# Kernel optimization log

Measured on AMD Instinct MI355X. Metric: run time of the kernel, lower is better.

The kernel has to match this reference:

```python
import jax, jax.numpy as jnp
import numpy as np

N_NODES = 100000
N_EDGES = 3200000
F_IN = 512
HIDDEN = 16
N_LABELS = 64


def _degree_norms(edge_src, edge_dst, n):
    # DGL GraphConv norm='both': src side uses out-degree, dst side uses in-degree,
    # both clamped to min 1, raised to -1/2.
    ones = jnp.ones(edge_src.shape[0], dtype=jnp.float32)
    deg_out = jax.ops.segment_sum(ones, edge_src, num_segments=n)
    deg_in = jax.ops.segment_sum(ones, edge_dst, num_segments=n)
    norm_src = jax.lax.rsqrt(jnp.maximum(deg_out, 1.0))
    norm_dst = jax.lax.rsqrt(jnp.maximum(deg_in, 1.0))
    return norm_src, norm_dst


def setup_inputs() -> dict:
    key = jax.random.key(0)
    k_x, k_s, k_d, k_w1, k_b1, k_w2, k_b2 = jax.random.split(key, 7)
    features = jax.random.normal(k_x, (N_NODES, F_IN), dtype=jnp.float32)
    edge_src = jax.random.randint(k_s, (N_EDGES,), 0, N_NODES, dtype=jnp.int64)
    edge_dst = jax.random.randint(k_d, (N_EDGES,), 0, N_NODES, dtype=jnp.int64)
    # GraphConv params (glorot-ish scale)
    W1 = jax.random.normal(k_w1, (F_IN, HIDDEN), dtype=jnp.float32) * (1.0 / np.sqrt(F_IN))
    b1 = jnp.zeros((HIDDEN,), dtype=jnp.float32)
    W2 = jax.random.normal(k_w2, (HIDDEN, N_LABELS), dtype=jnp.float32) * (1.0 / np.sqrt(HIDDEN))
    b2 = jnp.zeros((N_LABELS,), dtype=jnp.float32)
    return {"features": features, "W1": W1, "b1": b1, "W2": W2, "b2": b2,
            "edge_src": edge_src, "edge_dst": edge_dst}


def reference(features, W1, b1, W2, b2, edge_src, edge_dst):
    n = features.shape[0]
    norm_src, norm_dst = _degree_norms(edge_src, edge_dst, n)

    # Layer 1: in_feats (512) > out_feats (16) -> DGL projects first, then aggregates.
    h = features * norm_src[:, None]          # [N, 512]
    h = h @ W1                                 # [N, 16]
    h = jax.ops.segment_sum(h[edge_src], edge_dst, num_segments=n)  # SpMM gather+scatter
    h = h * norm_dst[:, None] + b1
    h = jax.nn.relu(h)  # GraphConv activation; outer F.relu is idempotent

    # Layer 2: in_feats (16) <= out_feats (64) -> DGL aggregates first, then projects.
    h2 = h * norm_src[:, None]                 # [N, 16]
    h2 = jax.ops.segment_sum(h2[edge_src], edge_dst, num_segments=n)
    h2 = h2 * norm_dst[:, None]
    out = h2 @ W2 + b2                          # [N, 64]
    return out
```

## Files before the change

### kernel.cpp

```cpp
#include <hip/hip_runtime.h>

#define N_NODES 100000
#define N_EDGES 3200000
#define F_IN 512
#define HIDDEN 16
#define N_LABELS 64

#define BW 128
#define NBUCK ((N_NODES + BW - 1) / BW)
#define NCB 256
#define SCAN_N (NBUCK * NCB)
#define SCAN_BLKS ((SCAN_N + 1023) / 1024)
#define CAP 10240

__global__ __launch_bounds__(256) void count_kernel(
        const int* __restrict__ es, const int* __restrict__ ed,
        int* __restrict__ Msrc, int* __restrict__ Mdst) {
    __shared__ int h1[NBUCK], h2[NBUCK];
    const int tid = threadIdx.x, g = blockIdx.x;
    for (int i = tid; i < NBUCK; i += 256) { h1[i] = 0; h2[i] = 0; }
    __syncthreads();
    for (int i = g * 256 + tid; i < N_EDGES; i += NCB * 256) {
        atomicAdd(&h1[es[i] >> 7], 1);
        atomicAdd(&h2[ed[i] >> 7], 1);
    }
    __syncthreads();
    for (int i = tid; i < NBUCK; i += 256) {
        Msrc[i * NCB + g] = h1[i];
        Mdst[i * NCB + g] = h2[i];
    }
}

__global__ __launch_bounds__(256) void scanA_kernel(int* __restrict__ a, int* __restrict__ bsum) {
    __shared__ int s[256];
    const int tid = threadIdx.x;
    const int base = blockIdx.x * 1024 + tid * 4;
    int4 v = make_int4(0, 0, 0, 0);
    if (base + 3 < SCAN_N) v = *(const int4*)(a + base);
    else {
        if (base + 0 < SCAN_N) v.x = a[base + 0];
        if (base + 1 < SCAN_N) v.y = a[base + 1];
        if (base + 2 < SCAN_N) v.z = a[base + 2];
        if (base + 3 < SCAN_N) v.w = a[base + 3];
    }
    const int lsum = v.x + v.y + v.z + v.w;
    s[tid] = lsum;
    __syncthreads();
    for (int off = 1; off < 256; off <<= 1) {
        int t = (tid >= off) ? s[tid - off] : 0;
        __syncthreads();
        s[tid] += t;
        __syncthreads();
    }
    int e0 = s[tid] - lsum;
    int e1 = e0 + v.x, e2 = e1 + v.y, e3 = e2 + v.z;
    if (base + 3 < SCAN_N) *(int4*)(a + base) = make_int4(e0, e1, e2, e3);
    else {
        if (base + 0 < SCAN_N) a[base + 0] = e0;
        if (base + 1 < SCAN_N) a[base + 1] = e1;
        if (base + 2 < SCAN_N) a[base + 2] = e2;
        if (base + 3 < SCAN_N) a[base + 3] = e3;
    }
    if (tid == 255) bsum[blockIdx.x] = s[255];
}

__global__ void scanB_kernel(int* __restrict__ bsum) {
    __shared__ int s[256];
    const int tid = threadIdx.x;
    int v = (tid < SCAN_BLKS) ? bsum[tid] : 0;
    s[tid] = v;
    __syncthreads();
    for (int off = 1; off < 256; off <<= 1) {
        int t = (tid >= off) ? s[tid - off] : 0;
        __syncthreads();
        s[tid] += t;
        __syncthreads();
    }
    if (tid < SCAN_BLKS) bsum[tid] = s[tid] - v;
}

__global__ __launch_bounds__(256) void scanC_kernel(int* __restrict__ a, const int* __restrict__ bsum) {
    const int base = blockIdx.x * 1024 + threadIdx.x * 4;
    const int b = bsum[blockIdx.x];
    if (base + 3 < SCAN_N) {
        int4 v = *(int4*)(a + base);
        v.x += b; v.y += b; v.z += b; v.w += b;
        *(int4*)(a + base) = v;
    } else {
        for (int j = 0; j < 4; ++j) if (base + j < SCAN_N) a[base + j] += b;
    }
}

__global__ __launch_bounds__(256) void scatter_kernel(
        const int* __restrict__ es, const int* __restrict__ ed,
        const int* __restrict__ Ssrc, const int* __restrict__ Sdst,
        unsigned* __restrict__ pairs, unsigned char* __restrict__ srcb) {
    __shared__ int c1[NBUCK], c2[NBUCK];
    const int tid = threadIdx.x, g = blockIdx.x;
    for (int i = tid; i < NBUCK; i += 256) {
        c1[i] = Ssrc[i * NCB + g];
        c2[i] = Sdst[i * NCB + g];
    }
    __syncthreads();
    for (int i = g * 256 + tid; i < N_EDGES; i += NCB * 256) {
        int s = es[i], d = ed[i];
        int p2 = atomicAdd(&c2[d >> 7], 1);
        pairs[p2] = ((unsigned)(d & 127) << 17) | (unsigned)s;
        int p1 = atomicAdd(&c1[s >> 7], 1);
        srcb[p1] = (unsigned char)(s & 127);
    }
}

__global__ __launch_bounds__(256) void csr_kernel(
        const int* __restrict__ Sdst, unsigned* __restrict__ pairs,
        int* __restrict__ row_ptr, float* __restrict__ norm_dst) {
    __shared__ unsigned buf[CAP];
    __shared__ int hist[BW], scn[BW], cur[BW];
    const int b = blockIdx.x, tid = threadIdx.x;
    const int base  = Sdst[b * NCB];
    const int nextb = (b == NBUCK - 1) ? N_EDGES : Sdst[(b + 1) * NCB];
    const int nb = nextb - base;
    const bool fits = (nb <= CAP);
    if (tid < BW) hist[tid] = 0;
    __syncthreads();
    for (int i = tid; i < nb; i += 256) {
        unsigned pk = pairs[base + i];
        if (fits) buf[i] = pk;
        atomicAdd(&hist[pk >> 17], 1);
    }
    __syncthreads();
    if (tid < BW) scn[tid] = hist[tid];
    __syncthreads();
    for (int off = 1; off < BW; off <<= 1) {
        int t = 0;
        if (tid < BW && tid >= off) t = scn[tid - off];
        __syncthreads();
        if (tid < BW) scn[tid] += t;
        __syncthreads();
    }
    if (tid < BW) {
        int e = scn[tid] - hist[tid];
        cur[tid] = e;
        int node = b * BW + tid;
        if (node <= N_NODES) row_ptr[node] = base + e;
        if (node < N_NODES) norm_dst[node] = rsqrtf(fmaxf((float)hist[tid], 1.0f));
    }
    __syncthreads();
    if (fits) {
        for (int i = tid; i < nb; i += 256) {
            unsigned pk = buf[i];
            int pos = atomicAdd(&cur[pk >> 17], 1);
            pairs[base + pos] = pk & 0x1FFFFu;
        }
    } else {
        for (int i = tid; i < nb; i += 256)
            pairs[base + i] &= 0x1FFFFu;
    }
}

__global__ __launch_bounds__(256) void srcdeg_kernel(
        const int* __restrict__ Ssrc, const unsigned char* __restrict__ srcb,
        float* __restrict__ norm_src) {
    __shared__ int hist[BW];
    const int b = blockIdx.x, tid = threadIdx.x;
    const int base  = Ssrc[b * NCB];
    const int nextb = (b == NBUCK - 1) ? N_EDGES : Ssrc[(b + 1) * NCB];
    const int nb = nextb - base;
    if (tid < BW) hist[tid] = 0;
    __syncthreads();
    for (int i = tid; i < nb; i += 256)
        atomicAdd(&hist[srcb[base + i]], 1);
    __syncthreads();
    if (tid < BW) {
        int node = b * BW + tid;
        if (node < N_NODES) norm_src[node] = rsqrtf(fmaxf((float)hist[tid], 1.0f));
    }
}

#define P1_ROWS 256
#define P1_CH 32
#define KSPLIT 2
#define KH (F_IN / KSPLIT)
#define P1_CHUNKS (KH / P1_CH)
#define P1_BLKS ((N_NODES + P1_ROWS - 1) / P1_ROWS)

#define GLD16(gp, lp) __builtin_amdgcn_global_load_lds( \
    (const __attribute__((address_space(1))) unsigned int*)(gp), \
    (__attribute__((address_space(3))) unsigned int*)(lp), 16, 0, 0)

__global__ __launch_bounds__(256, 2) void proj1_kernel(
        const float* __restrict__ X, const float* __restrict__ W1,
        float* __restrict__ P0, float* __restrict__ P1) {
    __shared__ float xs[2][P1_ROWS * P1_CH];
    __shared__ float w1c[KH * HIDDEN];

    const int tid = threadIdx.x;
    const int node0 = blockIdx.x * P1_ROWS;
    const int z = blockIdx.y;

    const int srow0 = tid >> 3;
    const int scg   = tid & 7;
    const int wbase = tid & 192;

    for (int i = tid; i < KH * HIDDEN / 4; i += 256)
        ((float4*)w1c)[i] = ((const float4*)(W1 + (size_t)z * KH * HIDDEN))[i];

    {
        const float* Xc = X + (size_t)z * KH;
#pragma unroll
        for (int it = 0; it < 8; ++it) {
            int row = srow0 + it * 32;
            int grow = node0 + row;
            if (grow > N_NODES - 1) grow = N_NODES - 1;
            int cg = scg ^ ((row >> 2) & 7);
            const float* gp = Xc + (size_t)grow * F_IN + cg * 4;
            float* lp = &xs[0][(size_t)(it * 256 + wbase) * 4];
            GLD16(gp, lp);
        }
    }
    __syncthreads();

    const int rg = tid >> 2;
    const int kq = (tid & 3) * 4;

    float acc[4][4];
#pragma unroll
    for (int a = 0; a < 4; ++a)
#pragma unroll
        for (int b = 0; b < 4; ++b) acc[a][b] = 0.f;

    for (int cc = 0; cc < P1_CHUNKS; ++cc) {
        const int cur = cc & 1;

        if (cc + 1 < P1_CHUNKS) {
            const float* Xc = X + (size_t)z * KH + (size_t)(cc + 1) * P1_CH;
#pragma unroll
            for (int it = 0; it < 8; ++it) {
                int row = srow0 + it * 32;
                int grow = node0 + row;
                if (grow > N_NODES - 1) grow = N_NODES - 1;
                int cg = scg ^ ((row >> 2) & 7);
                const float* gp = Xc + (size_t)grow * F_IN + cg * 4;
                float* lp = &xs[cur ^ 1][(size_t)(it * 256 + wbase) * 4];
                GLD16(gp, lp);
            }
        }

        const float* xb = &xs[cur][0];
#pragma unroll
        for (int kk4 = 0; kk4 < 8; ++kk4) {
            float4 w0 = *((const float4*)&w1c[(cc * P1_CH + kk4 * 4 + 0) * HIDDEN + kq]);
            float4 w1 = *((const float4*)&w1c[(cc * P1_CH + kk4 * 4 + 1) * HIDDEN + kq]);
            float4 w2 = *((const float4*)&w1c[(cc * P1_CH + kk4 * 4 + 2) * HIDDEN + kq]);
            float4 w3 = *((const float4*)&w1c[(cc * P1_CH + kk4 * 4 + 3) * HIDDEN + kq]);
#pragma unroll
            for (int a = 0; a < 4; ++a) {
                int row = rg * 4 + a;
                int sw  = (row >> 2) & 7;
                float4 xv = *((const float4*)&xb[row * P1_CH + ((kk4 ^ sw) * 4)]);
                acc[a][0] += xv.x * w0.x; acc[a][1] += xv.x * w0.y;
                acc[a][2] += xv.x * w0.z; acc[a][3] += xv.x * w0.w;
                acc[a][0] += xv.y * w1.x; acc[a][1] += xv.y * w1.y;
                acc[a][2] += xv.y * w1.z; acc[a][3] += xv.y * w1.w;
                acc[a][0] += xv.z * w2.x; acc[a][1] += xv.z * w2.y;
                acc[a][2] += xv.z * w2.z; acc[a][3] += xv.z * w2.w;
                acc[a][0] += xv.w * w3.x; acc[a][1] += xv.w * w3.y;
                acc[a][2] += xv.w * w3.z; acc[a][3] += xv.w * w3.w;
            }
        }

        __syncthreads();
    }

    float* Pz = z ? P1 : P0;
#pragma unroll
    for (int a = 0; a < 4; ++a) {
        int gn = node0 + rg * 4 + a;
        if (gn < N_NODES)
            *((float4*)(Pz + (size_t)gn * HIDDEN + kq)) =
                make_float4(acc[a][0], acc[a][1], acc[a][2], acc[a][3]);
    }
}

__global__ void reduce1_kernel(const float* __restrict__ P0, const float* __restrict__ P1,
                               const float* __restrict__ norm_src, float* __restrict__ H1) {
    int gid = blockIdx.x * blockDim.x + threadIdx.x;
    if (gid < N_NODES * 4) {
        float4 a = ((const float4*)P0)[gid];
        float4 b = ((const float4*)P1)[gid];
        float ns = norm_src[gid >> 2];
        ((float4*)H1)[gid] = make_float4((a.x + b.x) * ns, (a.y + b.y) * ns,
                                         (a.z + b.z) * ns, (a.w + b.w) * ns);
    }
}

__global__ __launch_bounds__(256) void spmm1_kernel(
        const int* __restrict__ rp, const int* __restrict__ col,
        const float* __restrict__ H1, const float* __restrict__ norm_dst,
        const float* __restrict__ norm_src, const float* __restrict__ b1,
        float* __restrict__ H1b) {
    int tid = threadIdx.x;
    int node = blockIdx.x * 16 + (tid >> 4);
    int k = tid & 15;
    if (node >= N_NODES) return;
    int beg = rp[node], end = rp[node + 1];
    float acc = 0.f;
    int j = beg;
    for (; j + 3 < end; j += 4) {
        int s0 = col[j], s1 = col[j + 1], s2 = col[j + 2], s3 = col[j + 3];
        float v0 = H1[(size_t)s0 * HIDDEN + k];
        float v1 = H1[(size_t)s1 * HIDDEN + k];
        float v2 = H1[(size_t)s2 * HIDDEN + k];
        float v3 = H1[(size_t)s3 * HIDDEN + k];
        acc += v0 + v1 + v2 + v3;
    }
    for (; j < end; ++j) acc += H1[(size_t)col[j] * HIDDEN + k];
    float v = fmaxf(acc * norm_dst[node] + b1[k], 0.f) * norm_src[node];
    H1b[(size_t)node * HIDDEN + k] = v;
}

__global__ __launch_bounds__(256) void spmm2_final_kernel(
        const int* __restrict__ rp, const int* __restrict__ col,
        const float* __restrict__ H1b, const float* __restrict__ norm_dst,
        const float* __restrict__ W2, const float* __restrict__ b2,
        float* __restrict__ out) {
    __shared__ float w2s[HIDDEN * N_LABELS];
    int tid = threadIdx.x;
    ((float4*)w2s)[tid] = ((const float4*)W2)[tid];
    __syncthreads();

    int node = blockIdx.x * 16 + (tid >> 4);
    int k = tid & 15;
    if (node >= N_NODES) return;
    int beg = rp[node], end = rp[node + 1];
    float acc = 0.f;
    int j = beg;
    for (; j + 3 < end; j += 4) {
        int s0 = col[j], s1 = col[j + 1], s2 = col[j + 2], s3 = col[j + 3];
        float v0 = H1b[(size_t)s0 * HIDDEN + k];
        float v1 = H1b[(size_t)s1 * HIDDEN + k];
        float v2 = H1b[(size_t)s2 * HIDDEN + k];
        float v3 = H1b[(size_t)s3 * HIDDEN + k];
        acc += v0 + v1 + v2 + v3;
    }
    for (; j < end; ++j) acc += H1b[(size_t)col[j] * HIDDEN + k];
    acc *= norm_dst[node];

    float4 o = ((const float4*)b2)[k];
#pragma unroll
    for (int jj = 0; jj < HIDDEN; ++jj) {
        float hj = __shfl(acc, jj, 16);
        float4 w = *((const float4*)&w2s[jj * N_LABELS + 4 * k]);
        o.x += hj * w.x; o.y += hj * w.y; o.z += hj * w.z; o.w += hj * w.w;
    }
    ((float4*)out)[(size_t)node * 16 + k] = o;
}

extern "C" void kernel_launch(void* const* d_in, const int* in_sizes, int n_in,
                              void* d_out, int out_size, void* d_ws, size_t ws_size,
                              hipStream_t stream) {
    const float* X  = (const float*)d_in[0];
    const float* W1 = (const float*)d_in[1];
    const float* b1 = (const float*)d_in[2];
    const float* W2 = (const float*)d_in[3];
    const float* b2 = (const float*)d_in[4];
    const int* es   = (const int*)d_in[5];
    const int* ed   = (const int*)d_in[6];
    float* out = (float*)d_out;

    char* ws = (char*)d_ws;
    float* norm_src = (float*)ws;  ws += (size_t)N_NODES * 4;
    float* norm_dst = (float*)ws;  ws += (size_t)N_NODES * 4;
    int*   row_ptr  = (int*)ws;    ws += 400016;
    char*  R1 = ws;                ws += (size_t)N_NODES * HIDDEN * 4;
    char*  R2 = ws;                ws += (size_t)N_NODES * HIDDEN * 4;
    char*  R3 = ws;

    unsigned char* srcb = (unsigned char*)R1;
    float* P0  = (float*)R1;
    float* H1  = (float*)R1;
    int*   Sdst = (int*)R2;
    int*   Ssrc = (int*)(R2 + 800768);
    int*   bs1  = (int*)(R2 + 1601536);
    int*   bs2  = (int*)(R2 + 1602560);
    float* P1   = (float*)R2;
    float* H1b  = (float*)R2;
    unsigned* pairs = (unsigned*)R3;
    int*   col  = (int*)R3;

    count_kernel<<<NCB, 256, 0, stream>>>(es, ed, Ssrc, Sdst);
    scanA_kernel<<<SCAN_BLKS, 256, 0, stream>>>(Sdst, bs1);
    scanA_kernel<<<SCAN_BLKS, 256, 0, stream>>>(Ssrc, bs2);
    scanB_kernel<<<1, 256, 0, stream>>>(bs1);
    scanB_kernel<<<1, 256, 0, stream>>>(bs2);
    scanC_kernel<<<SCAN_BLKS, 256, 0, stream>>>(Sdst, bs1);
    scanC_kernel<<<SCAN_BLKS, 256, 0, stream>>>(Ssrc, bs2);
    scatter_kernel<<<NCB, 256, 0, stream>>>(es, ed, Ssrc, Sdst, pairs, srcb);
    csr_kernel<<<NBUCK, 256, 0, stream>>>(Sdst, pairs, row_ptr, norm_dst);
    srcdeg_kernel<<<NBUCK, 256, 0, stream>>>(Ssrc, srcb, norm_src);
    proj1_kernel<<<dim3(P1_BLKS, KSPLIT), 256, 0, stream>>>(X, W1, P0, P1);
    reduce1_kernel<<<(N_NODES * 4 + 255) / 256, 256, 0, stream>>>(P0, P1, norm_src, H1);
    spmm1_kernel<<<(N_NODES + 15) / 16, 256, 0, stream>>>(row_ptr, col, H1, norm_dst, norm_src, b1, H1b);
    spmm2_final_kernel<<<(N_NODES + 15) / 16, 256, 0, stream>>>(row_ptr, col, H1b, norm_dst, W2, b2, out);
}
```

Baseline: 598.8 us.

## Merge scan launches, widen histogram blocks, retile projection to 128 rows x 64 cols

Pairs of scan kernels for the src and dst histograms are merged into single launches using a second grid dimension, cutting launch count. Count and scatter kernels move to 512 threads per block. The first-layer projection is retiled to 128 rows per block with 64-column chunks, two rows per thread and a new swizzle, doubling the grid and skipping the final barrier. Fewer rows per thread lowers register pressure but halves weight reuse per thread, and the scatter ordering within each bucket changes.

```diff
diff --git a/kernel.cpp b/kernel.cpp
--- a/kernel.cpp
+++ b/kernel.cpp
@@ -13,25 +13,29 @@
 #define SCAN_BLKS ((SCAN_N + 1023) / 1024)
 #define CAP 10240
 
-__global__ __launch_bounds__(256) void count_kernel(
+__global__ __launch_bounds__(512) void count_kernel(
         const int* __restrict__ es, const int* __restrict__ ed,
         int* __restrict__ Msrc, int* __restrict__ Mdst) {
     __shared__ int h1[NBUCK], h2[NBUCK];
     const int tid = threadIdx.x, g = blockIdx.x;
-    for (int i = tid; i < NBUCK; i += 256) { h1[i] = 0; h2[i] = 0; }
-    __syncthreads();
-    for (int i = g * 256 + tid; i < N_EDGES; i += NCB * 256) {
+    for (int i = tid; i < NBUCK; i += 512) { h1[i] = 0; h2[i] = 0; }
+    __syncthreads();
+    for (int i = g * 512 + tid; i < N_EDGES; i += NCB * 512) {
         atomicAdd(&h1[es[i] >> 7], 1);
         atomicAdd(&h2[ed[i] >> 7], 1);
     }
     __syncthreads();
-    for (int i = tid; i < NBUCK; i += 256) {
+    for (int i = tid; i < NBUCK; i += 512) {
         Msrc[i * NCB + g] = h1[i];
         Mdst[i * NCB + g] = h2[i];
     }
 }
 
-__global__ __launch_bounds__(256) void scanA_kernel(int* __restrict__ a, int* __restrict__ bsum) {
+__global__ __launch_bounds__(256) void scanA_kernel(
+        int* __restrict__ a0, int* __restrict__ a1,
+        int* __restrict__ b0, int* __restrict__ b1) {
+    int* a    = blockIdx.y ? a1 : a0;
+    int* bsum = blockIdx.y ? b1 : b0;
     __shared__ int s[256];
     const int tid = threadIdx.x;
     const int base = blockIdx.x * 1024 + tid * 4;
@@ -64,7 +68,8 @@
     if (tid == 255) bsum[blockIdx.x] = s[255];
 }
 
-__global__ void scanB_kernel(int* __restrict__ bsum) {
+__global__ void scanB_kernel(int* __restrict__ b0, int* __restrict__ b1) {
+    int* bsum = blockIdx.y ? b1 : b0;
     __shared__ int s[256];
     const int tid = threadIdx.x;
     int v = (tid < SCAN_BLKS) ? bsum[tid] : 0;
@@ -79,7 +84,11 @@
     if (tid < SCAN_BLKS) bsum[tid] = s[tid] - v;
 }
 
-__global__ __launch_bounds__(256) void scanC_kernel(int* __restrict__ a, const int* __restrict__ bsum) {
+__global__ __launch_bounds__(256) void scanC_kernel(
+        int* __restrict__ a0, int* __restrict__ a1,
+        const int* __restrict__ b0, const int* __restrict__ b1) {
+    int* a = blockIdx.y ? a1 : a0;
+    const int* bsum = blockIdx.y ? b1 : b0;
     const int base = blockIdx.x * 1024 + threadIdx.x * 4;
     const int b = bsum[blockIdx.x];
     if (base + 3 < SCAN_N) {
@@ -91,18 +100,18 @@
     }
 }
 
-__global__ __launch_bounds__(256) void scatter_kernel(
+__global__ __launch_bounds__(512) void scatter_kernel(
         const int* __restrict__ es, const int* __restrict__ ed,
         const int* __restrict__ Ssrc, const int* __restrict__ Sdst,
         unsigned* __restrict__ pairs, unsigned char* __restrict__ srcb) {
     __shared__ int c1[NBUCK], c2[NBUCK];
     const int tid = threadIdx.x, g = blockIdx.x;
-    for (int i = tid; i < NBUCK; i += 256) {
+    for (int i = tid; i < NBUCK; i += 512) {
         c1[i] = Ssrc[i * NCB + g];
         c2[i] = Sdst[i * NCB + g];
     }
     __syncthreads();
-    for (int i = g * 256 + tid; i < N_EDGES; i += NCB * 256) {
+    for (int i = g * 512 + tid; i < N_EDGES; i += NCB * 512) {
         int s = es[i], d = ed[i];
         int p2 = atomicAdd(&c2[d >> 7], 1);
         pairs[p2] = ((unsigned)(d & 127) << 17) | (unsigned)s;
@@ -177,8 +186,8 @@
     }
 }
 
-#define P1_ROWS 256
-#define P1_CH 32
+#define P1_ROWS 128
+#define P1_CH 64
 #define KSPLIT 2
 #define KH (F_IN / KSPLIT)
 #define P1_CHUNKS (KH / P1_CH)
@@ -187,6 +196,22 @@
 #define GLD16(gp, lp) __builtin_amdgcn_global_load_lds( \
     (const __attribute__((address_space(1))) unsigned int*)(gp), \
     (__attribute__((address_space(3))) unsigned int*)(lp), 16, 0, 0)
+
+__device__ __forceinline__ void p1_stage(const float* __restrict__ Xz,
+                                         int node0, int cc, float* lbuf,
+                                         int tid) {
+    const int wbase = tid & 192;
+#pragma unroll
+    for (int it = 0; it < 8; ++it) {
+        int row = it * 16 + (tid >> 4);
+        int grow = node0 + row;
+        if (grow > N_NODES - 1) grow = N_NODES - 1;
+        int cg = (tid & 15) ^ ((row >> 1) & 7);
+        const float* gp = Xz + (size_t)grow * F_IN + cc * P1_CH + cg * 4;
+        float* lp = lbuf + (size_t)(it * 256 + wbase) * 4;
+        GLD16(gp, lp);
+    }
+}
 
 __global__ __launch_bounds__(256, 2) void proj1_kernel(
         const float* __restrict__ X, const float* __restrict__ W1,
@@ -197,67 +222,40 @@
     const int tid = threadIdx.x;
     const int node0 = blockIdx.x * P1_ROWS;
     const int z = blockIdx.y;
-
-    const int srow0 = tid >> 3;
-    const int scg   = tid & 7;
-    const int wbase = tid & 192;
+    const float* Xz = X + (size_t)z * KH;
 
     for (int i = tid; i < KH * HIDDEN / 4; i += 256)
         ((float4*)w1c)[i] = ((const float4*)(W1 + (size_t)z * KH * HIDDEN))[i];
 
-    {
-        const float* Xc = X + (size_t)z * KH;
-#pragma unroll
-        for (int it = 0; it < 8; ++it) {
-            int row = srow0 + it * 32;
-            int grow = node0 + row;
-            if (grow > N_NODES - 1) grow = N_NODES - 1;
-            int cg = scg ^ ((row >> 2) & 7);
-            const float* gp = Xc + (size_t)grow * F_IN + cg * 4;
-            float* lp = &xs[0][(size_t)(it * 256 + wbase) * 4];
-            GLD16(gp, lp);
-        }
-    }
+    p1_stage(Xz, node0, 0, &xs[0][0], tid);
     __syncthreads();
 
     const int rg = tid >> 2;
     const int kq = (tid & 3) * 4;
-
-    float acc[4][4];
-#pragma unroll
-    for (int a = 0; a < 4; ++a)
+    const int sw = rg & 7;
+
+    float acc[2][4];
+#pragma unroll
+    for (int a = 0; a < 2; ++a)
 #pragma unroll
         for (int b = 0; b < 4; ++b) acc[a][b] = 0.f;
 
     for (int cc = 0; cc < P1_CHUNKS; ++cc) {
-        const int cur = cc & 1;
-
-        if (cc + 1 < P1_CHUNKS) {
-            const float* Xc = X + (size_t)z * KH + (size_t)(cc + 1) * P1_CH;
-#pragma unroll
-            for (int it = 0; it < 8; ++it) {
-                int row = srow0 + it * 32;
-                int grow = node0 + row;
-                if (grow > N_NODES - 1) grow = N_NODES - 1;
-                int cg = scg ^ ((row >> 2) & 7);
-                const float* gp = Xc + (size_t)grow * F_IN + cg * 4;
-                float* lp = &xs[cur ^ 1][(size_t)(it * 256 + wbase) * 4];
-                GLD16(gp, lp);
-            }
-        }
-
-        const float* xb = &xs[cur][0];
-#pragma unroll
-        for (int kk4 = 0; kk4 < 8; ++kk4) {
-            float4 w0 = *((const float4*)&w1c[(cc * P1_CH + kk4 * 4 + 0) * HIDDEN + kq]);
-            float4 w1 = *((const float4*)&w1c[(cc * P1_CH + kk4 * 4 + 1) * HIDDEN + kq]);
-            float4 w2 = *((const float4*)&w1c[(cc * P1_CH + kk4 * 4 + 2) * HIDDEN + kq]);
-            float4 w3 = *((const float4*)&w1c[(cc * P1_CH + kk4 * 4 + 3) * HIDDEN + kq]);
-#pragma unroll
-            for (int a = 0; a < 4; ++a) {
-                int row = rg * 4 + a;
-                int sw  = (row >> 2) & 7;
-                float4 xv = *((const float4*)&xb[row * P1_CH + ((kk4 ^ sw) * 4)]);
+        if (cc + 1 < P1_CHUNKS)
+            p1_stage(Xz, node0, cc + 1, &xs[(cc & 1) ^ 1][0], tid);
+
+        const float* xb = &xs[cc & 1][0];
+#pragma unroll
+        for (int j = 0; j < 16; ++j) {
+            const int k = cc * P1_CH + j * 4;
+            float4 w0 = *((const float4*)&w1c[(k + 0) * HIDDEN + kq]);
+            float4 w1 = *((const float4*)&w1c[(k + 1) * HIDDEN + kq]);
+            float4 w2 = *((const float4*)&w1c[(k + 2) * HIDDEN + kq]);
+            float4 w3 = *((const float4*)&w1c[(k + 3) * HIDDEN + kq]);
+#pragma unroll
+            for (int a = 0; a < 2; ++a) {
+                int row = rg * 2 + a;
+                float4 xv = *((const float4*)&xb[row * P1_CH + ((j ^ sw) * 4)]);
                 acc[a][0] += xv.x * w0.x; acc[a][1] += xv.x * w0.y;
                 acc[a][2] += xv.x * w0.z; acc[a][3] += xv.x * w0.w;
                 acc[a][0] += xv.y * w1.x; acc[a][1] += xv.y * w1.y;
@@ -269,13 +267,14 @@
             }
         }
 
-        __syncthreads();
+        if (cc + 1 < P1_CHUNKS)
+            __syncthreads();
     }
 
     float* Pz = z ? P1 : P0;
 #pragma unroll
-    for (int a = 0; a < 4; ++a) {
-        int gn = node0 + rg * 4 + a;
+    for (int a = 0; a < 2; ++a) {
+        int gn = node0 + rg * 2 + a;
         if (gn < N_NODES)
             *((float4*)(Pz + (size_t)gn * HIDDEN + kq)) =
                 make_float4(acc[a][0], acc[a][1], acc[a][2], acc[a][3]);
@@ -388,14 +387,11 @@
     unsigned* pairs = (unsigned*)R3;
     int*   col  = (int*)R3;
 
-    count_kernel<<<NCB, 256, 0, stream>>>(es, ed, Ssrc, Sdst);
-    scanA_kernel<<<SCAN_BLKS, 256, 0, stream>>>(Sdst, bs1);
-    scanA_kernel<<<SCAN_BLKS, 256, 0, stream>>>(Ssrc, bs2);
-    scanB_kernel<<<1, 256, 0, stream>>>(bs1);
-    scanB_kernel<<<1, 256, 0, stream>>>(bs2);
-    scanC_kernel<<<SCAN_BLKS, 256, 0, stream>>>(Sdst, bs1);
-    scanC_kernel<<<SCAN_BLKS, 256, 0, stream>>>(Ssrc, bs2);
-    scatter_kernel<<<NCB, 256, 0, stream>>>(es, ed, Ssrc, Sdst, pairs, srcb);
+    count_kernel<<<NCB, 512, 0, stream>>>(es, ed, Ssrc, Sdst);
+    scanA_kernel<<<dim3(SCAN_BLKS, 2), 256, 0, stream>>>(Sdst, Ssrc, bs1, bs2);
+    scanB_kernel<<<dim3(1, 2), 256, 0, stream>>>(bs1, bs2);
+    scanC_kernel<<<dim3(SCAN_BLKS, 2), 256, 0, stream>>>(Sdst, Ssrc, bs1, bs2);
+    scatter_kernel<<<NCB, 512, 0, stream>>>(es, ed, Ssrc, Sdst, pairs, srcb);
     csr_kernel<<<NBUCK, 256, 0, stream>>>(Sdst, pairs, row_ptr, norm_dst);
     srcdeg_kernel<<<NBUCK, 256, 0, stream>>>(Ssrc, srcb, norm_src);
     proj1_kernel<<<dim3(P1_BLKS, KSPLIT), 256, 0, stream>>>(X, W1, P0, P1);
```

New measurement: 625.4 us. 1.04x slower.
